# Kernel optimization log

Measured on AMD Instinct MI355X. Metric: run time of the kernel, lower is better.

Reference implementation:

```python
import jax, jax.numpy as jnp
import numpy as np

B, T, D, H = 16, 81, 128, 8  # batch, ntok, d_model (= d_head), n_head


def setup_inputs() -> dict:
    key = jax.random.key(0)
    ks = jax.random.split(key, 6)
    s = 0.02
    return {
        "x": jax.random.normal(ks[0], (B, T, D), jnp.float32),
        "msk": jnp.ones((1, H, T, T), jnp.float32),
        "wqkv_w": jax.random.normal(ks[1], (H * 2 * D, D), jnp.float32) * s,
        "wqkv_b": jax.random.normal(ks[2], (H * 2 * D,), jnp.float32) * s,
        "wk_w": jax.random.normal(ks[3], (H, D), jnp.float32) * s,
        "fanout_w": jax.random.normal(ks[4], (D, D), jnp.float32) * s,
        "fanout_b": jax.random.normal(ks[5], (D,), jnp.float32) * s,
        "head_enabled": jnp.ones((H,), jnp.float32),
        "n": 0, "layer": 0, "pas": 1,
    }


def quick_gelu(x):
    return x * jax.nn.sigmoid(1.702 * x)


def reference(x, msk, wqkv_w, wqkv_b, wk_w, fanout_w, fanout_b, head_enabled, n, layer, pas):
    b, t, d = x.shape
    h = wk_w.shape[0]
    # qkv projection: per-head q and v of full width d (d_head == d_model)
    y = x @ wqkv_w.T + wqkv_b                      # [b, t, h*2*d]
    y = y.reshape(b, t, h, 2 * d)
    q, v = y[..., :d], y[..., d:]                  # [b, t, h, d] each
    # k: input gated per-head by wk.weight rows
    k = x[:, :, None, :] * wk_w[None, None, :, :]  # [b, t, h, d]
    # v gating by head-enabled flags
    v = v * head_enabled[None, None, :, None]
    # L1 attention scores: a[b,h,t,s] = -sum_d |q[b,t,h,d] - k[b,s,h,d]| / sqrt(d)
    diff = jnp.abs(q[:, :, None, :, :] - k[:, None, :, :, :])  # [b, t, s, h, d]
    a = -diff.sum(-1)                               # [b, t, s, h]
    a = jnp.transpose(a, (0, 3, 1, 2)) / jnp.sqrt(jnp.asarray(d, x.dtype))  # [b,h,t,s]
    a = jax.nn.softmax(a, axis=3) * msk
    bo = jnp.einsum('bhts,bshd->bthd', a, v)        # [b, t, h, d]
    bo = bo.sum(axis=2)                             # sum over heads -> [b, t, d]
    ap = jnp.transpose(a[0] - 1.0 + msk[0], (1, 2, 0))  # [t, s, h]
    z = quick_gelu(bo + 4.0) - 4.0
    z = z @ fanout_w.T + fanout_b
    return (x + z, ap)
```

## Files before the change

kernel.cpp:

```cpp
#include <hip/hip_runtime.h>
#include <math.h>

#define Bq 16
#define Tq 81
#define Dq 128
#define Hq 8
#define BT (Bq*Tq)
#define BTD (Bq*Tq*Dq)
#define PS 84
#define P_SZ   (Bq*Tq*Hq*PS)
#define QV_SZ  (BT*Hq*Dq)
#define P_OFF  0
#define Q_OFF  (P_OFF + P_SZ)
#define V_OFF  (Q_OFF + QV_SZ)
#define XB_OFF (V_OFF + QV_SZ)
#define XB_FSZ (BTD/2)
#define WB_OFF (XB_OFF + XB_FSZ)

typedef __attribute__((ext_vector_type(8))) short short8;
typedef __attribute__((ext_vector_type(4))) float f32x4;

__device__ __forceinline__ float l1_4(const float4 q, const float4 k) {
    return fabsf(q.x - k.x) + fabsf(q.y - k.y) + fabsf(q.z - k.z) + fabsf(q.w - k.w);
}
__device__ __forceinline__ int imin(int a, int b) { return a < b ? a : b; }
__device__ __forceinline__ unsigned short f2bf(float f) {
    unsigned u = __float_as_uint(f);
    u += 0x7fffu + ((u >> 16) & 1u);
    return (unsigned short)(u >> 16);
}

__global__ __launch_bounds__(256) void k_prep(
    const float* __restrict__ w, const float* __restrict__ x,
    unsigned short* __restrict__ Wb, unsigned short* __restrict__ xb)
{
    const int NW4 = (Hq * 2 * Dq * Dq) / 4;
    const int NX4 = BTD / 4;
    const int idx = blockIdx.x * 256 + threadIdx.x;
    if (idx < NW4) {
        const float4 v = ((const float4*)w)[idx];
        ushort4 o;
        o.x = f2bf(v.x); o.y = f2bf(v.y); o.z = f2bf(v.z); o.w = f2bf(v.w);
        ((ushort4*)Wb)[idx] = o;
    } else if (idx < NW4 + NX4) {
        const int j = idx - NW4;
        const float4 v = ((const float4*)x)[j];
        ushort4 o;
        o.x = f2bf(v.x); o.y = f2bf(v.y); o.z = f2bf(v.z); o.w = f2bf(v.w);
        ((ushort4*)xb)[j] = o;
    }
}

__global__ __launch_bounds__(256) void k_qkv_mfma(
    const unsigned short* __restrict__ xb, const unsigned short* __restrict__ Wb,
    const float* __restrict__ bias, const float* __restrict__ he,
    float* __restrict__ Qo, float* __restrict__ Vo)
{
    const int tid = threadIdx.x;
    const int w = tid >> 6, lane = tid & 63;
    const int ln = lane & 15, quad = lane >> 4;
    const int mt = blockIdx.x * 4 + w;
    const int n0 = blockIdx.y * 64;
    const int h  = blockIdx.y >> 2;
    const int isV = (blockIdx.y >> 1) & 1;
    const int c0 = (blockIdx.y & 1) * 64;

    const int row = mt * 16 + ln;
    const int arow = row < BT ? row : BT - 1;
    const unsigned short* xa  = xb + (size_t)arow * Dq + quad * 8;
    const unsigned short* wb0 = Wb + (size_t)(n0 + ln) * Dq + quad * 8;

    f32x4 acc[4];
    #pragma unroll
    for (int i = 0; i < 4; ++i) acc[i] = (f32x4){0.f, 0.f, 0.f, 0.f};

    #pragma unroll
    for (int kb = 0; kb < Dq; kb += 32) {
        const short8 af = *(const short8*)(xa + kb);
        #pragma unroll
        for (int nt = 0; nt < 4; ++nt) {
            const short8 bf = *(const short8*)(wb0 + (size_t)(nt * 16) * Dq + kb);
            acc[nt] = __builtin_amdgcn_mfma_f32_16x16x32_bf16(af, bf, acc[nt], 0, 0, 0);
        }
    }

    if (mt >= 81) return;
    const float scale = isV ? he[h] : 1.0f;
    float* dst = isV ? Vo : Qo;
    const int gm0 = mt * 16 + quad * 4;
    #pragma unroll
    for (int nt = 0; nt < 4; ++nt) {
        const float bn = bias[n0 + nt * 16 + ln];
        #pragma unroll
        for (int r = 0; r < 4; ++r) {
            const int gm = gm0 + r;
            const int bb = gm / 81, tt = gm - bb * 81;
            dst[(((size_t)bb * Hq + h) * Tq + tt) * Dq + c0 + nt * 16 + ln] =
                (acc[nt][r] + bn) * scale;
        }
    }
}

__global__ __launch_bounds__(256) void k_scores(
    const float* __restrict__ x, const float* __restrict__ Q,
    const float* __restrict__ wk, const float* __restrict__ msk,
    float* __restrict__ P, float* __restrict__ out)
{
    __shared__ float Kl[81 * 132];
    __shared__ float sc[21 * 85];
    __shared__ float rsum[24];
    const int tid = threadIdx.x;
    const int tq = blockIdx.x, h = blockIdx.y, b = blockIdx.z;
    const int t0g = tq * 21;
    const int nt = (tq == 3) ? 18 : 21;

    {
        const float* wkb = wk + (size_t)h * Dq;
        for (int idx = tid; idx < Tq * 32; idx += 256) {
            const int r = idx >> 5, c = idx & 31;
            const float4 xv = *(const float4*)(x + (size_t)(b * Tq + r) * Dq + c * 4);
            const float4 wv = *(const float4*)(wkb + c * 4);
            float4 kv;
            kv.x = xv.x * wv.x; kv.y = xv.y * wv.y;
            kv.z = xv.z * wv.z; kv.w = xv.w * wv.w;
            *(float4*)(&Kl[r * 132 + c * 4]) = kv;
        }
    }
    __syncthreads();

    if (tid < 147) {
        const int tg = tid / 21, sg = tid % 21;
        const float* qrow[3];
        #pragma unroll
        for (int i = 0; i < 3; ++i) {
            const int t = imin(t0g + tg * 3 + i, Tq - 1);
            qrow[i] = Q + (((size_t)b * Hq + h) * Tq + t) * Dq;
        }
        int sidx[4];
        #pragma unroll
        for (int j = 0; j < 4; ++j) sidx[j] = imin(sg + 21 * j, Tq - 1);

        float acc[3][4];
        #pragma unroll
        for (int i = 0; i < 3; ++i)
            #pragma unroll
            for (int j = 0; j < 4; ++j) acc[i][j] = 0.f;

        #pragma unroll 2
        for (int k4 = 0; k4 < 32; ++k4) {
            float4 kv[4];
            #pragma unroll
            for (int j = 0; j < 4; ++j)
                kv[j] = *(const float4*)(&Kl[sidx[j] * 132 + k4 * 4]);
            #pragma unroll
            for (int i = 0; i < 3; ++i) {
                const float4 qv = *(const float4*)(qrow[i] + k4 * 4);
                #pragma unroll
                for (int j = 0; j < 4; ++j)
                    acc[i][j] += l1_4(qv, kv[j]);
            }
        }
        const float ns = -0.08838834764831845f;
        #pragma unroll
        for (int i = 0; i < 3; ++i) {
            const int tl = tg * 3 + i;
            #pragma unroll
            for (int j = 0; j < 4; ++j)
                sc[tl * 85 + sg + 21 * j] = acc[i][j] * ns;
        }
    }
    __syncthreads();

    {
        const int w = tid >> 6, lane = tid & 63;
        for (int r = w; r < nt; r += 4) {
            float* row = sc + r * 85;
            const bool hi = (lane + 64) < Tq;
            const float v0 = row[lane];
            const float v1 = hi ? row[lane + 64] : -1e30f;
            float m = fmaxf(v0, v1);
            #pragma unroll
            for (int off = 32; off > 0; off >>= 1)
                m = fmaxf(m, __shfl_xor(m, off));
            const float e0 = __expf(v0 - m);
            const float e1 = hi ? __expf(v1 - m) : 0.f;
            float s = e0 + e1;
            #pragma unroll
            for (int off = 32; off > 0; off >>= 1)
                s += __shfl_xor(s, off);
            row[lane] = e0;
            if (hi) row[lane + 64] = e1;
            if (lane == 0) rsum[r] = 1.0f / s;
        }
    }
    __syncthreads();

    const bool doap = (b == 0);
    for (int idx = tid; idx < nt * Tq; idx += 256) {
        const int tl = idx / Tq, s = idx - tl * Tq;
        const int tg2 = t0g + tl;
        const float mv = msk[((size_t)h * Tq + tg2) * Tq + s];
        const float pm = sc[tl * 85 + s] * rsum[tl] * mv;
        P[(((size_t)b * Tq + tg2) * Hq + h) * PS + s] = pm;
        if (doap) out[BTD + ((size_t)tg2 * Tq + s) * Hq + h] = pm - 1.0f + mv;
    }
}

__global__ __launch_bounds__(512) void k_out(
    const float* __restrict__ x, const float* __restrict__ P,
    const float* __restrict__ V, const float* __restrict__ fw,
    const float* __restrict__ fb, float* __restrict__ out)
{
    __shared__ float Pl[8][Hq][PS];
    __shared__ float bo_part[8][8][128];
    __shared__ float zs[8][128];
    const int tid = threadIdx.x;
    const int t0 = blockIdx.x * 8, b = blockIdx.y;

    {
        const float4* src = (const float4*)(P + ((size_t)b * Tq + t0) * Hq * PS);
        #pragma unroll
        for (int idx = tid; idx < 8 * Hq * PS / 4; idx += 512)
            ((float4*)Pl)[idx] = src[idx];
    }
    __syncthreads();

    const int w = tid >> 6, lane = tid & 63;
    {
        const int d0 = lane * 2;
        float2 acc[8];
        #pragma unroll
        for (int i = 0; i < 8; ++i) acc[i] = make_float2(0.f, 0.f);
        const float* vp = V + (((size_t)b * Hq + w) * Tq) * Dq + d0;
        for (int s4 = 0; s4 < 20; ++s4) {
            float4 p[8];
            #pragma unroll
            for (int t = 0; t < 8; ++t)
                p[t] = *(const float4*)(&Pl[t][w][s4 * 4]);
            #pragma unroll
            for (int ss = 0; ss < 4; ++ss) {
                const int s = s4 * 4 + ss;
                const float2 vv = *(const float2*)(vp + (size_t)s * Dq);
                #pragma unroll
                for (int t = 0; t < 8; ++t) {
                    const float pv = ((const float*)&p[t])[ss];
                    acc[t].x = fmaf(pv, vv.x, acc[t].x);
                    acc[t].y = fmaf(pv, vv.y, acc[t].y);
                }
            }
        }
        {
            const float2 vv = *(const float2*)(vp + (size_t)80 * Dq);
            #pragma unroll
            for (int t = 0; t < 8; ++t) {
                const float pv = Pl[t][w][80];
                acc[t].x = fmaf(pv, vv.x, acc[t].x);
                acc[t].y = fmaf(pv, vv.y, acc[t].y);
            }
        }
        #pragma unroll
        for (int t = 0; t < 8; ++t) {
            bo_part[w][t][d0]     = acc[t].x;
            bo_part[w][t][d0 + 1] = acc[t].y;
        }
    }
    __syncthreads();

    #pragma unroll
    for (int idx = tid; idx < 1024; idx += 512) {
        const int t = idx >> 7, d = idx & 127;
        float bo = 0.f;
        #pragma unroll
        for (int ww = 0; ww < 8; ++ww) bo += bo_part[ww][t][d];
        const float tt = bo + 4.0f;
        const float sg = 1.0f / (1.0f + __expf(-1.702f * tt));
        zs[t][d] = tt * sg - 4.0f;
    }
    __syncthreads();

    {
        const int n = tid & 127, tg = tid >> 7;
        const float* fwr = fw + (size_t)n * Dq;
        const float fbn = fb[n];
        float a0 = 0.f, a1 = 0.f;
        #pragma unroll 8
        for (int k4 = 0; k4 < 32; ++k4) {
            const float4 w4 = *(const float4*)(fwr + k4 * 4);
            const float4 z0 = *(const float4*)(&zs[tg][k4 * 4]);
            const float4 z1 = *(const float4*)(&zs[tg + 4][k4 * 4]);
            a0 += z0.x * w4.x + z0.y * w4.y + z0.z * w4.z + z0.w * w4.w;
            a1 += z1.x * w4.x + z1.y * w4.y + z1.z * w4.z + z1.w * w4.w;
        }
        const int t1 = t0 + tg, t2 = t0 + tg + 4;
        if (t1 < Tq) {
            const size_t o = ((size_t)b * Tq + t1) * Dq + n;
            out[o] = x[o] + a0 + fbn;
        }
        if (t2 < Tq) {
            const size_t o = ((size_t)b * Tq + t2) * Dq + n;
            out[o] = x[o] + a1 + fbn;
        }
    }
}

extern "C" void kernel_launch(void* const* d_in, const int* in_sizes, int n_in,
                              void* d_out, int out_size, void* d_ws, size_t ws_size,
                              hipStream_t stream) {
    const float* x        = (const float*)d_in[0];
    const float* msk      = (const float*)d_in[1];
    const float* wqkv_w   = (const float*)d_in[2];
    const float* wqkv_b   = (const float*)d_in[3];
    const float* wk_w     = (const float*)d_in[4];
    const float* fanout_w = (const float*)d_in[5];
    const float* fanout_b = (const float*)d_in[6];
    const float* he       = (const float*)d_in[7];
    float* out = (float*)d_out;
    float* ws  = (float*)d_ws;

    float* P   = ws + P_OFF;
    float* Q   = ws + Q_OFF;
    float* V   = ws + V_OFF;
    unsigned short* xb = (unsigned short*)(ws + XB_OFF);
    unsigned short* Wb = (unsigned short*)(ws + WB_OFF);

    k_prep<<<dim3(418), 256, 0, stream>>>(wqkv_w, x, Wb, xb);
    k_qkv_mfma<<<dim3(21, 32), 256, 0, stream>>>(xb, Wb, wqkv_b, he, Q, V);
    k_scores<<<dim3(4, 8, 16), 256, 0, stream>>>(x, Q, wk_w, msk, P, out);
    k_out<<<dim3(11, 16), 512, 0, stream>>>(x, P, V, fanout_w, fanout_b, out);
}
```

Before: 130.7 us.

## Fuse bf16 conversion into QKV MFMA kernel and retile L1 score loop

Drops the separate prep kernel that converted weights and activations to bf16, and converts fp32 loads to bf16 inside the MFMA projection kernel instead. This removes one launch and a write/read pass over the converted buffers, at the cost of reading twice the bytes and redundant conversion work across blocks. Separately, the L1 score kernel is retiled so 243 threads each compute 7 query rows against one key row, instead of 147 threads each doing a 3x4 tile. This changes the balance between register reuse and thread count.

New measurement: 135.3 us. 3.5% more time.

```diff
diff --git a/kernel.cpp b/kernel.cpp
--- a/kernel.cpp
+++ b/kernel.cpp
@@ -13,9 +13,6 @@
 #define P_OFF  0
 #define Q_OFF  (P_OFF + P_SZ)
 #define V_OFF  (Q_OFF + QV_SZ)
-#define XB_OFF (V_OFF + QV_SZ)
-#define XB_FSZ (BTD/2)
-#define WB_OFF (XB_OFF + XB_FSZ)
 
 typedef __attribute__((ext_vector_type(8))) short short8;
 typedef __attribute__((ext_vector_type(4))) float f32x4;
@@ -29,30 +26,17 @@
     u += 0x7fffu + ((u >> 16) & 1u);
     return (unsigned short)(u >> 16);
 }
-
-__global__ __launch_bounds__(256) void k_prep(
-    const float* __restrict__ w, const float* __restrict__ x,
-    unsigned short* __restrict__ Wb, unsigned short* __restrict__ xb)
-{
-    const int NW4 = (Hq * 2 * Dq * Dq) / 4;
-    const int NX4 = BTD / 4;
-    const int idx = blockIdx.x * 256 + threadIdx.x;
-    if (idx < NW4) {
-        const float4 v = ((const float4*)w)[idx];
-        ushort4 o;
-        o.x = f2bf(v.x); o.y = f2bf(v.y); o.z = f2bf(v.z); o.w = f2bf(v.w);
-        ((ushort4*)Wb)[idx] = o;
-    } else if (idx < NW4 + NX4) {
-        const int j = idx - NW4;
-        const float4 v = ((const float4*)x)[j];
-        ushort4 o;
-        o.x = f2bf(v.x); o.y = f2bf(v.y); o.z = f2bf(v.z); o.w = f2bf(v.w);
-        ((ushort4*)xb)[j] = o;
-    }
+__device__ __forceinline__ short8 cvt8(const float4 a, const float4 b) {
+    short8 r;
+    r[0] = (short)f2bf(a.x); r[1] = (short)f2bf(a.y);
+    r[2] = (short)f2bf(a.z); r[3] = (short)f2bf(a.w);
+    r[4] = (short)f2bf(b.x); r[5] = (short)f2bf(b.y);
+    r[6] = (short)f2bf(b.z); r[7] = (short)f2bf(b.w);
+    return r;
 }
 
 __global__ __launch_bounds__(256) void k_qkv_mfma(
-    const unsigned short* __restrict__ xb, const unsigned short* __restrict__ Wb,
+    const float* __restrict__ x, const float* __restrict__ wqkv,
     const float* __restrict__ bias, const float* __restrict__ he,
     float* __restrict__ Qo, float* __restrict__ Vo)
 {
@@ -67,8 +51,8 @@
 
     const int row = mt * 16 + ln;
     const int arow = row < BT ? row : BT - 1;
-    const unsigned short* xa  = xb + (size_t)arow * Dq + quad * 8;
-    const unsigned short* wb0 = Wb + (size_t)(n0 + ln) * Dq + quad * 8;
+    const float* xa = x + (size_t)arow * Dq + quad * 8;
+    const float* wb0 = wqkv + (size_t)(n0 + ln) * Dq + quad * 8;
 
     f32x4 acc[4];
     #pragma unroll
@@ -76,10 +60,13 @@
 
     #pragma unroll
     for (int kb = 0; kb < Dq; kb += 32) {
-        const short8 af = *(const short8*)(xa + kb);
+        const short8 af = cvt8(*(const float4*)(xa + kb),
+                               *(const float4*)(xa + kb + 4));
         #pragma unroll
         for (int nt = 0; nt < 4; ++nt) {
-            const short8 bf = *(const short8*)(wb0 + (size_t)(nt * 16) * Dq + kb);
+            const float* wr = wb0 + (size_t)(nt * 16) * Dq + kb;
+            const short8 bf = cvt8(*(const float4*)(wr),
+                                   *(const float4*)(wr + 4));
             acc[nt] = __builtin_amdgcn_mfma_f32_16x16x32_bf16(af, bf, acc[nt], 0, 0, 0);
         }
     }
@@ -128,46 +115,31 @@
     }
     __syncthreads();
 
-    if (tid < 147) {
-        const int tg = tid / 21, sg = tid % 21;
-        const float* qrow[3];
-        #pragma unroll
-        for (int i = 0; i < 3; ++i) {
-            const int t = imin(t0g + tg * 3 + i, Tq - 1);
+    if (tid < 243) {
+        const int tg = tid / 81, sg = tid % 81;
+        const float* qrow[7];
+        #pragma unroll
+        for (int i = 0; i < 7; ++i) {
+            const int t = imin(t0g + tg * 7 + i, Tq - 1);
             qrow[i] = Q + (((size_t)b * Hq + h) * Tq + t) * Dq;
         }
-        int sidx[4];
-        #pragma unroll
-        for (int j = 0; j < 4; ++j) sidx[j] = imin(sg + 21 * j, Tq - 1);
-
-        float acc[3][4];
-        #pragma unroll
-        for (int i = 0; i < 3; ++i)
-            #pragma unroll
-            for (int j = 0; j < 4; ++j) acc[i][j] = 0.f;
-
-        #pragma unroll 2
+        float acc[7];
+        #pragma unroll
+        for (int i = 0; i < 7; ++i) acc[i] = 0.f;
+
+        #pragma unroll 4
         for (int k4 = 0; k4 < 32; ++k4) {
-            float4 kv[4];
-            #pragma unroll
-            for (int j = 0; j < 4; ++j)
-                kv[j] = *(const float4*)(&Kl[sidx[j] * 132 + k4 * 4]);
-            #pragma unroll
-            for (int i = 0; i < 3; ++i) {
+            const float4 kv = *(const float4*)(&Kl[sg * 132 + k4 * 4]);
+            #pragma unroll
+            for (int i = 0; i < 7; ++i) {
                 const float4 qv = *(const float4*)(qrow[i] + k4 * 4);
-                #pragma unroll
-                for (int j = 0; j < 4; ++j)
-                    acc[i][j] += l1_4(qv, kv[j]);
+                acc[i] += l1_4(qv, kv);
             }
         }
         const float ns = -0.08838834764831845f;
         #pragma unroll
-        for (int i = 0; i < 3; ++i) {
-            const int tl = tg * 3 + i;
-            #pragma unroll
-            for (int j = 0; j < 4; ++j)
-                sc[tl * 85 + sg + 21 * j] = acc[i][j] * ns;
-        }
+        for (int i = 0; i < 7; ++i)
+            sc[(tg * 7 + i) * 85 + sg] = acc[i] * ns;
     }
     __syncthreads();
 
@@ -320,11 +292,8 @@
     float* P   = ws + P_OFF;
     float* Q   = ws + Q_OFF;
     float* V   = ws + V_OFF;
-    unsigned short* xb = (unsigned short*)(ws + XB_OFF);
-    unsigned short* Wb = (unsigned short*)(ws + WB_OFF);
-
-    k_prep<<<dim3(418), 256, 0, stream>>>(wqkv_w, x, Wb, xb);
-    k_qkv_mfma<<<dim3(21, 32), 256, 0, stream>>>(xb, Wb, wqkv_b, he, Q, V);
+
+    k_qkv_mfma<<<dim3(21, 32), 256, 0, stream>>>(x, wqkv_w, wqkv_b, he, Q, V);
     k_scores<<<dim3(4, 8, 16), 256, 0, stream>>>(x, Q, wk_w, msk, P, out);
     k_out<<<dim3(11, 16), 512, 0, stream>>>(x, P, V, fanout_w, fanout_b, out);
 }
```
